# Performance work log

Hardware: AMD Instinct MI355X
Metric: run time of the kernel (lower is better)

## Reference

```python
import jax, jax.numpy as jnp
import numpy as np

N_NODES = 25000
N_EDGES = 400000
CHANNELS = 32
EDGE_FEAT_DIM = 8
HIDDEN = 64
NUM_IRREPS = 4  # messages irreps = 2x0e + 2x1o -> 4 irreps, dim 8
AVG_NUM_NEIGHBORS = 16.0


def _mlp(x, W0, W1, W2, W3):
    # e3nn MultiLayerPerceptron: dense layers with 1/sqrt(fan_in) forward
    # normalization, silu on hidden layers, no output activation.
    for W in (W0, W1, W2):
        x = jax.nn.silu(x @ (W / jnp.sqrt(jnp.float32(W.shape[0]))))
    return x @ (W3 / jnp.sqrt(jnp.float32(W3.shape[0])))


def setup_inputs() -> dict:
    key = jax.random.key(0)
    ks = jax.random.split(key, 9)
    node_feats = jax.random.normal(ks[0], (N_NODES, CHANNELS, 4), jnp.float32)
    edge_attrs = jax.random.normal(ks[1], (N_EDGES, 4), jnp.float32)
    edge_feats = jax.random.normal(ks[2], (N_EDGES, EDGE_FEAT_DIM), jnp.float32)
    senders = jax.random.randint(ks[3], (N_EDGES,), 0, N_NODES)
    receivers = jax.random.randint(ks[4], (N_EDGES,), 0, N_NODES)
    W0 = jax.random.normal(ks[5], (EDGE_FEAT_DIM, HIDDEN), jnp.float32)
    W1 = jax.random.normal(ks[6], (HIDDEN, HIDDEN), jnp.float32)
    W2 = jax.random.normal(ks[7], (HIDDEN, HIDDEN), jnp.float32)
    W3 = jax.random.normal(ks[8], (HIDDEN, CHANNELS * NUM_IRREPS), jnp.float32)
    return {"node_feats": node_feats, "edge_attrs": edge_attrs,
            "edge_feats": edge_feats, "senders": senders, "receivers": receivers,
            "W0": W0, "W1": W1, "W2": W2, "W3": W3}


def reference(node_feats, edge_attrs, edge_feats, senders, receivers, W0, W1, W2, W3):
    # Gather sender node features: [E, C, 4] with irreps 0e (dim1) + 1o (dim3)
    x = node_feats[senders]
    s, v = x[..., 0], x[..., 1:4]            # [E,C], [E,C,3]
    a_s = edge_attrs[:, 0]                   # Y_0: [E]
    a_v = edge_attrs[:, 1:4]                 # Y_1: [E,3]

    # CG tensor product filtered to 0e + 1o (e3nn normalization: sqrt(2l3+1)*w3j)
    m0a = s * a_s[:, None]                                   # 0e x 0e -> 0e  [E,C]
    m0b = jnp.einsum('ecd,ed->ec', v, a_v) / jnp.sqrt(3.0)   # 1o x 1o -> 0e  [E,C]
    m1a = s[..., None] * a_v[:, None, :]                     # 0e x 1o -> 1o  [E,C,3]
    m1b = v * a_s[:, None, None]                             # 1o x 0e -> 1o  [E,C,3]

    # Edge MLP gate: [E, C*num_irreps] -> mul_to_axis -> [E, C, num_irreps]
    mix = _mlp(edge_feats, W0, W1, W2, W3).reshape(N_EDGES, CHANNELS, NUM_IRREPS)

    # Elementwise tensor product with 4x0e scalars: per-irrep gating
    out_s = jnp.stack([m0a * mix[..., 0], m0b * mix[..., 1]], axis=-1)          # [E,C,2]
    out_v = jnp.concatenate([m1a * mix[..., 2:3], m1b * mix[..., 3:4]], axis=-1)  # [E,C,6]
    messages = jnp.concatenate([out_s, out_v], axis=-1)                          # [E,C,8]

    # Scatter-add into receivers, then normalize by sqrt(avg_num_neighbors)
    agg = jax.ops.segment_sum(messages, receivers, num_segments=N_NODES)
    return agg / jnp.sqrt(AVG_NUM_NEIGHBORS)
```

## Files before the change

kernel.cpp:

```cpp
#include <hip/hip_runtime.h>
#include <hip/hip_fp16.h>

#define NE 400000
#define NN 25000
#define MAXDEG 56
#define LDS_STRIDE 65

typedef __attribute__((ext_vector_type(8))) _Float16 half8;
typedef __attribute__((ext_vector_type(4))) _Float16 half4;
typedef __attribute__((ext_vector_type(4))) float f32x4;

#define WS_MIX_OFF   0ull
#define WS_SLOTS_OFF 102400000ull
#define WS_CNT_OFF   108000000ull
#define WS_WBUF_OFF  108100000ull
#define WS_NEED      108136864ull

#define WB_L0 0
#define WB_L1 2048
#define WB_L2 6144
#define WB_L3 10240

__device__ __forceinline__ float fast_silu(float x) {
    float e = __expf(-x);
    return x * __builtin_amdgcn_rcpf(1.0f + e);
}

__global__ __launch_bounds__(64) void prep_weights(
    const float* __restrict__ W0, const float* __restrict__ W1,
    const float* __restrict__ W2, const float* __restrict__ W3,
    _Float16* __restrict__ wbuf, int* __restrict__ cnt)
{
    const int f    = blockIdx.x;
    const int lane = threadIdx.x;

    for (int i = f * 64 + lane; i < NN; i += 36 * 64) cnt[i] = 0;

    const int n    = lane & 15;
    const int quad = lane >> 4;

    const float* W; int K, N, kt, nt, fl, base; float scale;
    if (f < 4)       { W = W0; K = 8;  N = 64;  fl = f;      kt = 0;       nt = fl;     scale = 0.35355339059327373f; base = WB_L0; }
    else if (f < 12) { W = W1; K = 64; N = 64;  fl = f - 4;  kt = fl >> 2; nt = fl & 3; scale = 0.125f;   base = WB_L1; }
    else if (f < 20) { W = W2; K = 64; N = 64;  fl = f - 12; kt = fl >> 2; nt = fl & 3; scale = 0.125f;   base = WB_L2; }
    else             { W = W3; K = 64; N = 128; fl = f - 20; kt = fl >> 3; nt = fl & 7; scale = 0.03125f; base = WB_L3; }

    _Float16 v[8];
    #pragma unroll
    for (int j = 0; j < 8; ++j) {
        const int k = kt * 32 + quad * 8 + j;
        const float val = (k < K) ? W[k * N + nt * 16 + n] * scale : 0.0f;
        v[j] = (_Float16)val;
    }
    *(half8*)(wbuf + base + fl * 512 + lane * 8) = *(const half8*)v;
}

#define HS 72
__global__ __launch_bounds__(256) void mlp_build_kernel(
    const float*    __restrict__ edge_feats,
    const int*      __restrict__ receivers,
    const _Float16* __restrict__ wbuf,
    int*            __restrict__ cnt,
    int*            __restrict__ slots,
    _Float16*       __restrict__ mix16)
{
    __shared__ _Float16 H[4 * 2 * 16 * HS];
    const int tid  = threadIdx.x;
    const int wave = tid >> 6;
    const int lane = tid & 63;
    const int col  = lane & 15;
    const int quad = lane >> 4;

    if (tid < 128) {
        const int e = blockIdx.x * 128 + tid;
        const int r = receivers[e];
        const int s = atomicAdd(&cnt[r], 1);
        if (s < MAXDEG) slots[r * MAXDEG + s] = e;
    }

    const int e0 = (blockIdx.x * 4 + wave) * 32;
    _Float16* HA = &H[wave * 2 * 16 * HS];
    _Float16* HB = HA + 16 * HS;
    const half8* wb = (const half8*)wbuf;
    const f32x4 zero4 = {0.f, 0.f, 0.f, 0.f};

    half8 b0A = {0, 0, 0, 0, 0, 0, 0, 0};
    half8 b0B = {0, 0, 0, 0, 0, 0, 0, 0};
    if (quad == 0) {
        const float4* pA = (const float4*)(edge_feats + (size_t)(e0 + col) * 8);
        const float4 xa = pA[0], ya = pA[1];
        b0A[0] = (_Float16)xa.x; b0A[1] = (_Float16)xa.y; b0A[2] = (_Float16)xa.z; b0A[3] = (_Float16)xa.w;
        b0A[4] = (_Float16)ya.x; b0A[5] = (_Float16)ya.y; b0A[6] = (_Float16)ya.z; b0A[7] = (_Float16)ya.w;
        const float4* pB = (const float4*)(edge_feats + (size_t)(e0 + 16 + col) * 8);
        const float4 xb = pB[0], yb = pB[1];
        b0B[0] = (_Float16)xb.x; b0B[1] = (_Float16)xb.y; b0B[2] = (_Float16)xb.z; b0B[3] = (_Float16)xb.w;
        b0B[4] = (_Float16)yb.x; b0B[5] = (_Float16)yb.y; b0B[6] = (_Float16)yb.z; b0B[7] = (_Float16)yb.w;
    }

    #pragma unroll
    for (int nt = 0; nt < 4; ++nt) {
        const half8 w = wb[(WB_L0 / 512 + nt) * 64 + lane];
        f32x4 aA = __builtin_amdgcn_mfma_f32_16x16x32_f16(w, b0A, zero4, 0, 0, 0);
        f32x4 aB = __builtin_amdgcn_mfma_f32_16x16x32_f16(w, b0B, zero4, 0, 0, 0);
        half4 hA, hB;
        #pragma unroll
        for (int r = 0; r < 4; ++r) { hA[r] = (_Float16)fast_silu(aA[r]); hB[r] = (_Float16)fast_silu(aB[r]); }
        *(half4*)&HA[col * HS + nt * 16 + quad * 4] = hA;
        *(half4*)&HB[col * HS + nt * 16 + quad * 4] = hB;
    }

    #pragma unroll
    for (int layer = 0; layer < 2; ++layer) {
        const int wbase = (layer == 0 ? WB_L1 : WB_L2) / 512;
        const half8 bloA = *(const half8*)&HA[col * HS + 0  + quad * 8];
        const half8 bhiA = *(const half8*)&HA[col * HS + 32 + quad * 8];
        const half8 bloB = *(const half8*)&HB[col * HS + 0  + quad * 8];
        const half8 bhiB = *(const half8*)&HB[col * HS + 32 + quad * 8];
        f32x4 aA[4], aB[4];
        #pragma unroll
        for (int nt = 0; nt < 4; ++nt) {
            const half8 wlo = wb[(wbase + 0 + nt) * 64 + lane];
            const half8 whi = wb[(wbase + 4 + nt) * 64 + lane];
            aA[nt] = __builtin_amdgcn_mfma_f32_16x16x32_f16(wlo, bloA, zero4, 0, 0, 0);
            aA[nt] = __builtin_amdgcn_mfma_f32_16x16x32_f16(whi, bhiA, aA[nt], 0, 0, 0);
            aB[nt] = __builtin_amdgcn_mfma_f32_16x16x32_f16(wlo, bloB, zero4, 0, 0, 0);
            aB[nt] = __builtin_amdgcn_mfma_f32_16x16x32_f16(whi, bhiB, aB[nt], 0, 0, 0);
        }
        #pragma unroll
        for (int nt = 0; nt < 4; ++nt) {
            half4 hA, hB;
            #pragma unroll
            for (int r = 0; r < 4; ++r) { hA[r] = (_Float16)fast_silu(aA[nt][r]); hB[r] = (_Float16)fast_silu(aB[nt][r]); }
            *(half4*)&HA[col * HS + nt * 16 + quad * 4] = hA;
            *(half4*)&HB[col * HS + nt * 16 + quad * 4] = hB;
        }
    }

    {
        const half8 bloA = *(const half8*)&HA[col * HS + 0  + quad * 8];
        const half8 bhiA = *(const half8*)&HA[col * HS + 32 + quad * 8];
        const half8 bloB = *(const half8*)&HB[col * HS + 0  + quad * 8];
        const half8 bhiB = *(const half8*)&HB[col * HS + 32 + quad * 8];
        _Float16* mrowA = mix16 + (size_t)(e0 + col) * 128;
        _Float16* mrowB = mix16 + (size_t)(e0 + 16 + col) * 128;
        #pragma unroll
        for (int nt = 0; nt < 8; ++nt) {
            const half8 wlo = wb[(WB_L3 / 512 + 0 + nt) * 64 + lane];
            const half8 whi = wb[(WB_L3 / 512 + 8 + nt) * 64 + lane];
            f32x4 aA = __builtin_amdgcn_mfma_f32_16x16x32_f16(wlo, bloA, zero4, 0, 0, 0);
            aA = __builtin_amdgcn_mfma_f32_16x16x32_f16(whi, bhiA, aA, 0, 0, 0);
            f32x4 aB = __builtin_amdgcn_mfma_f32_16x16x32_f16(wlo, bloB, zero4, 0, 0, 0);
            aB = __builtin_amdgcn_mfma_f32_16x16x32_f16(whi, bhiB, aB, 0, 0, 0);
            half4 hA, hB;
            #pragma unroll
            for (int r = 0; r < 4; ++r) { hA[r] = (_Float16)aA[r]; hB[r] = (_Float16)aB[r]; }
            *(half4*)&mrowA[nt * 16 + quad * 4] = hA;
            *(half4*)&mrowB[nt * 16 + quad * 4] = hB;
        }
    }
}

__global__ __launch_bounds__(64) void gather_kernel(
    const float*    __restrict__ node_feats,
    const float*    __restrict__ edge_attrs,
    const int*      __restrict__ senders,
    const _Float16* __restrict__ mix16,
    const int*      __restrict__ cnt,
    const int*      __restrict__ slots,
    float*          __restrict__ out)
{
    const int n    = blockIdx.x;
    const int lane = threadIdx.x;
    const int g    = lane >> 4;
    const int s    = lane & 15;
    const int c0   = 2 * s;
    const float inv_sqrt3 = 0.5773502691896258f;

    int d = cnt[n];
    if (d > MAXDEG) d = MAXDEG;
    const int* sl = slots + n * MAXDEG;

    float acc[16];
    #pragma unroll
    for (int j = 0; j < 16; ++j) acc[j] = 0.0f;

    #pragma unroll 2
    for (int base = 0; base < d; base += 4) {
        const int  ei  = base + g;
        const bool act = (ei < d);
        const int  eic = act ? ei : 0;
        const int  eid = sl[eic];
        const int  snd = senders[eid];
        const float4 a4v = ((const float4*)edge_attrs)[eid];
        const half8 m8 = *(const half8*)(mix16 + (size_t)eid * 128 + c0 * 4);
        const float4 xA = ((const float4*)(node_feats + (size_t)snd * 128))[c0];
        const float4 xB = ((const float4*)(node_feats + (size_t)snd * 128))[c0 + 1];

        const float z = act ? 1.0f : 0.0f;
        const float as = a4v.x, av0 = a4v.y, av1 = a4v.z, av2 = a4v.w;

        {
            const float m0 = z * (float)m8[0], m1 = z * (float)m8[1];
            const float m2 = z * (float)m8[2], m3 = z * (float)m8[3];
            const float sc = xA.x, v0 = xA.y, v1 = xA.z, v2 = xA.w;
            acc[0] = fmaf(sc * as, m0, acc[0]);
            const float dv = v0 * av0 + v1 * av1 + v2 * av2;
            acc[1] = fmaf(dv * inv_sqrt3, m1, acc[1]);
            acc[2] = fmaf(sc * av0, m2, acc[2]);
            acc[3] = fmaf(sc * av1, m2, acc[3]);
            acc[4] = fmaf(sc * av2, m2, acc[4]);
            acc[5] = fmaf(v0 * as, m3, acc[5]);
            acc[6] = fmaf(v1 * as, m3, acc[6]);
            acc[7] = fmaf(v2 * as, m3, acc[7]);
        }
        {
            const float m0 = z * (float)m8[4], m1 = z * (float)m8[5];
            const float m2 = z * (float)m8[6], m3 = z * (float)m8[7];
            const float sc = xB.x, v0 = xB.y, v1 = xB.z, v2 = xB.w;
            acc[8]  = fmaf(sc * as, m0, acc[8]);
            const float dv = v0 * av0 + v1 * av1 + v2 * av2;
            acc[9]  = fmaf(dv * inv_sqrt3, m1, acc[9]);
            acc[10] = fmaf(sc * av0, m2, acc[10]);
            acc[11] = fmaf(sc * av1, m2, acc[11]);
            acc[12] = fmaf(sc * av2, m2, acc[12]);
            acc[13] = fmaf(v0 * as, m3, acc[13]);
            acc[14] = fmaf(v1 * as, m3, acc[14]);
            acc[15] = fmaf(v2 * as, m3, acc[15]);
        }
    }

    #pragma unroll
    for (int j = 0; j < 16; ++j) {
        acc[j] += __shfl_xor(acc[j], 16, 64);
        acc[j] += __shfl_xor(acc[j], 32, 64);
    }

    if (g == 0) {
        float4* op = (float4*)(out + (size_t)n * 256 + s * 16);
        float4 r0; r0.x = acc[0];  r0.y = acc[1];  r0.z = acc[2];  r0.w = acc[3];
        float4 r1; r1.x = acc[4];  r1.y = acc[5];  r1.z = acc[6];  r1.w = acc[7];
        float4 r2; r2.x = acc[8];  r2.y = acc[9];  r2.z = acc[10]; r2.w = acc[11];
        float4 r3; r3.x = acc[12]; r3.y = acc[13]; r3.z = acc[14]; r3.w = acc[15];
        op[0] = r0; op[1] = r1; op[2] = r2; op[3] = r3;
    }
}

__global__ __launch_bounds__(128) void edge_mp_kernel(
    const float* __restrict__ node_feats, const float* __restrict__ edge_attrs,
    const float* __restrict__ edge_feats, const int* __restrict__ senders,
    const int* __restrict__ receivers, const float* __restrict__ W0,
    const float* __restrict__ W1, const float* __restrict__ W2,
    const float* __restrict__ W3, float* __restrict__ out)
{
    __shared__ float hbuf[128 * LDS_STRIDE];
    const int tid = threadIdx.x;
    const int e   = blockIdx.x * 128 + tid;
    if (e >= NE) return;
    float* hl = &hbuf[tid * LDS_STRIDE];

    float4 ef0 = ((const float4*)edge_feats)[e * 2 + 0];
    float4 ef1 = ((const float4*)edge_feats)[e * 2 + 1];
    float ef[8] = {ef0.x, ef0.y, ef0.z, ef0.w, ef1.x, ef1.y, ef1.z, ef1.w};
    float acc[64];
    #pragma unroll
    for (int i = 0; i < 64; ++i) acc[i] = 0.0f;
    #pragma unroll
    for (int j = 0; j < 8; ++j) {
        const float xj = ef[j];
        const float* wrow = W0 + j * 64;
        #pragma unroll
        for (int i = 0; i < 64; ++i) acc[i] = fmaf(xj, wrow[i], acc[i]);
    }
    {
        const float s0 = 0.35355339059327373f;
        #pragma unroll
        for (int i = 0; i < 64; ++i) hl[i] = fast_silu(acc[i] * s0);
    }
    #pragma unroll
    for (int i = 0; i < 64; ++i) acc[i] = 0.0f;
    #pragma unroll 4
    for (int j = 0; j < 64; ++j) {
        const float xj = hl[j];
        const float* wrow = W1 + j * 64;
        #pragma unroll
        for (int i = 0; i < 64; ++i) acc[i] = fmaf(xj, wrow[i], acc[i]);
    }
    #pragma unroll
    for (int i = 0; i < 64; ++i) hl[i] = fast_silu(acc[i] * 0.125f);
    #pragma unroll
    for (int i = 0; i < 64; ++i) acc[i] = 0.0f;
    #pragma unroll 4
    for (int j = 0; j < 64; ++j) {
        const float xj = hl[j];
        const float* wrow = W2 + j * 64;
        #pragma unroll
        for (int i = 0; i < 64; ++i) acc[i] = fmaf(xj, wrow[i], acc[i]);
    }
    float h2[64];
    #pragma unroll
    for (int i = 0; i < 64; ++i) h2[i] = fast_silu(acc[i] * 0.125f);

    const int snd = senders[e];
    const int rcv = receivers[e];
    const float4 a4 = ((const float4*)edge_attrs)[e];
    const float a_s = a4.x, av0 = a4.y, av1 = a4.z, av2 = a4.w;
    const float4* nf4 = (const float4*)(node_feats + (size_t)snd * 128);
    float* outp = out + (size_t)rcv * 256;
    const float mixscale = 0.03125f;
    const float inv_sqrt3 = 0.5773502691896258f;

    #pragma unroll 2
    for (int c = 0; c < 32; ++c) {
        float m0 = 0.0f, m1 = 0.0f, m2 = 0.0f, m3 = 0.0f;
        const float* wc = W3 + c * 4;
        #pragma unroll
        for (int j = 0; j < 64; ++j) {
            const float hj = h2[j];
            m0 = fmaf(hj, wc[j * 128 + 0], m0);
            m1 = fmaf(hj, wc[j * 128 + 1], m1);
            m2 = fmaf(hj, wc[j * 128 + 2], m2);
            m3 = fmaf(hj, wc[j * 128 + 3], m3);
        }
        m0 *= mixscale; m1 *= mixscale; m2 *= mixscale; m3 *= mixscale;
        const float4 x4 = nf4[c];
        const float s = x4.x, v0 = x4.y, v1 = x4.z, v2 = x4.w;
        float* op = outp + c * 8;
        atomicAdd(op + 0, s * a_s * m0);
        const float dotva = v0 * av0 + v1 * av1 + v2 * av2;
        atomicAdd(op + 1, dotva * inv_sqrt3 * m1);
        atomicAdd(op + 2, s * av0 * m2);
        atomicAdd(op + 3, s * av1 * m2);
        atomicAdd(op + 4, s * av2 * m2);
        atomicAdd(op + 5, v0 * a_s * m3);
        atomicAdd(op + 6, v1 * a_s * m3);
        atomicAdd(op + 7, v2 * a_s * m3);
    }
}

extern "C" void kernel_launch(void* const* d_in, const int* in_sizes, int n_in,
                              void* d_out, int out_size, void* d_ws, size_t ws_size,
                              hipStream_t stream) {
    const float* node_feats = (const float*)d_in[0];
    const float* edge_attrs = (const float*)d_in[1];
    const float* edge_feats = (const float*)d_in[2];
    const int*   senders    = (const int*)d_in[3];
    const int*   receivers  = (const int*)d_in[4];
    const float* W0 = (const float*)d_in[5];
    const float* W1 = (const float*)d_in[6];
    const float* W2 = (const float*)d_in[7];
    const float* W3 = (const float*)d_in[8];
    float* outp = (float*)d_out;

    if (ws_size >= WS_NEED) {
        char* w = (char*)d_ws;
        _Float16* mix16 = (_Float16*)(w + WS_MIX_OFF);
        int*      slots = (int*)(w + WS_SLOTS_OFF);
        int*      cnt   = (int*)(w + WS_CNT_OFF);
        _Float16* wbuf  = (_Float16*)(w + WS_WBUF_OFF);

        hipLaunchKernelGGL(prep_weights, dim3(36), dim3(64), 0, stream,
                           W0, W1, W2, W3, wbuf, cnt);
        hipLaunchKernelGGL(mlp_build_kernel, dim3(NE / 128), dim3(256), 0, stream,
                           edge_feats, receivers, wbuf, cnt, slots, mix16);
        hipLaunchKernelGGL(gather_kernel, dim3(NN), dim3(64), 0, stream,
                           node_feats, edge_attrs, senders, mix16, cnt, slots, outp);
    } else {
        hipMemsetAsync(d_out, 0, (size_t)out_size * sizeof(float), stream);
        hipLaunchKernelGGL(edge_mp_kernel, dim3((NE + 127) / 128), dim3(128), 0, stream,
                           node_feats, edge_attrs, edge_feats, senders, receivers,
                           W0, W1, W2, W3, outp);
    }
}
```

Baseline: 211.0 us.

## Make MLP kernel persistent with register-resident weights

The MLP/slot-building kernel becomes a persistent grid of 512 blocks that grid-stride over edge tiles and receiver-slot insertions. All 36 weight fragments are loaded into registers once per wave and reused across every tile, replacing per-tile weight reloads from global memory. Holding 36 half8 registers raises VGPR pressure, which the launch bound of 2 blocks per SM tries to contain. The cost is lower occupancy and possible load imbalance across the fixed grid.

After: 216.4 us. 1.03x slower.

```diff
diff --git a/kernel.cpp b/kernel.cpp
--- a/kernel.cpp
+++ b/kernel.cpp
@@ -5,6 +5,7 @@
 #define NN 25000
 #define MAXDEG 56
 #define LDS_STRIDE 65
+#define MLP_BLOCKS 512
 
 typedef __attribute__((ext_vector_type(8))) _Float16 half8;
 typedef __attribute__((ext_vector_type(4))) _Float16 half4;
@@ -56,7 +57,7 @@
 }
 
 #define HS 72
-__global__ __launch_bounds__(256) void mlp_build_kernel(
+__global__ __launch_bounds__(256, 2) void mlp_build_kernel(
     const float*    __restrict__ edge_feats,
     const int*      __restrict__ receivers,
     const _Float16* __restrict__ wbuf,
@@ -71,91 +72,93 @@
     const int col  = lane & 15;
     const int quad = lane >> 4;
 
-    if (tid < 128) {
-        const int e = blockIdx.x * 128 + tid;
+    for (int e = blockIdx.x * 256 + tid; e < NE; e += MLP_BLOCKS * 256) {
         const int r = receivers[e];
         const int s = atomicAdd(&cnt[r], 1);
         if (s < MAXDEG) slots[r * MAXDEG + s] = e;
     }
 
-    const int e0 = (blockIdx.x * 4 + wave) * 32;
+    const half8* wb = (const half8*)wbuf;
+    half8 w[36];
+    #pragma unroll
+    for (int i = 0; i < 36; ++i) w[i] = wb[i * 64 + lane];
+
     _Float16* HA = &H[wave * 2 * 16 * HS];
     _Float16* HB = HA + 16 * HS;
-    const half8* wb = (const half8*)wbuf;
     const f32x4 zero4 = {0.f, 0.f, 0.f, 0.f};
 
-    half8 b0A = {0, 0, 0, 0, 0, 0, 0, 0};
-    half8 b0B = {0, 0, 0, 0, 0, 0, 0, 0};
-    if (quad == 0) {
-        const float4* pA = (const float4*)(edge_feats + (size_t)(e0 + col) * 8);
-        const float4 xa = pA[0], ya = pA[1];
-        b0A[0] = (_Float16)xa.x; b0A[1] = (_Float16)xa.y; b0A[2] = (_Float16)xa.z; b0A[3] = (_Float16)xa.w;
-        b0A[4] = (_Float16)ya.x; b0A[5] = (_Float16)ya.y; b0A[6] = (_Float16)ya.z; b0A[7] = (_Float16)ya.w;
-        const float4* pB = (const float4*)(edge_feats + (size_t)(e0 + 16 + col) * 8);
-        const float4 xb = pB[0], yb = pB[1];
-        b0B[0] = (_Float16)xb.x; b0B[1] = (_Float16)xb.y; b0B[2] = (_Float16)xb.z; b0B[3] = (_Float16)xb.w;
-        b0B[4] = (_Float16)yb.x; b0B[5] = (_Float16)yb.y; b0B[6] = (_Float16)yb.z; b0B[7] = (_Float16)yb.w;
-    }
-
-    #pragma unroll
-    for (int nt = 0; nt < 4; ++nt) {
-        const half8 w = wb[(WB_L0 / 512 + nt) * 64 + lane];
-        f32x4 aA = __builtin_amdgcn_mfma_f32_16x16x32_f16(w, b0A, zero4, 0, 0, 0);
-        f32x4 aB = __builtin_amdgcn_mfma_f32_16x16x32_f16(w, b0B, zero4, 0, 0, 0);
-        half4 hA, hB;
-        #pragma unroll
-        for (int r = 0; r < 4; ++r) { hA[r] = (_Float16)fast_silu(aA[r]); hB[r] = (_Float16)fast_silu(aB[r]); }
-        *(half4*)&HA[col * HS + nt * 16 + quad * 4] = hA;
-        *(half4*)&HB[col * HS + nt * 16 + quad * 4] = hB;
-    }
-
-    #pragma unroll
-    for (int layer = 0; layer < 2; ++layer) {
-        const int wbase = (layer == 0 ? WB_L1 : WB_L2) / 512;
-        const half8 bloA = *(const half8*)&HA[col * HS + 0  + quad * 8];
-        const half8 bhiA = *(const half8*)&HA[col * HS + 32 + quad * 8];
-        const half8 bloB = *(const half8*)&HB[col * HS + 0  + quad * 8];
-        const half8 bhiB = *(const half8*)&HB[col * HS + 32 + quad * 8];
-        f32x4 aA[4], aB[4];
+    const int gw = blockIdx.x * 4 + wave;
+    for (int tp = gw; tp < NE / 32; tp += MLP_BLOCKS * 4) {
+        const int e0 = tp * 32;
+
+        half8 b0A = {0, 0, 0, 0, 0, 0, 0, 0};
+        half8 b0B = {0, 0, 0, 0, 0, 0, 0, 0};
+        if (quad == 0) {
+            const float4* pA = (const float4*)(edge_feats + (size_t)(e0 + col) * 8);
+            const float4 xa = pA[0], ya = pA[1];
+            b0A[0] = (_Float16)xa.x; b0A[1] = (_Float16)xa.y; b0A[2] = (_Float16)xa.z; b0A[3] = (_Float16)xa.w;
+            b0A[4] = (_Float16)ya.x; b0A[5] = (_Float16)ya.y; b0A[6] = (_Float16)ya.z; b0A[7] = (_Float16)ya.w;
+            const float4* pB = (const float4*)(edge_feats + (size_t)(e0 + 16 + col) * 8);
+            const float4 xb = pB[0], yb = pB[1];
+            b0B[0] = (_Float16)xb.x; b0B[1] = (_Float16)xb.y; b0B[2] = (_Float16)xb.z; b0B[3] = (_Float16)xb.w;
+            b0B[4] = (_Float16)yb.x; b0B[5] = (_Float16)yb.y; b0B[6] = (_Float16)yb.z; b0B[7] = (_Float16)yb.w;
+        }
+
         #pragma unroll
         for (int nt = 0; nt < 4; ++nt) {
-            const half8 wlo = wb[(wbase + 0 + nt) * 64 + lane];
-            const half8 whi = wb[(wbase + 4 + nt) * 64 + lane];
-            aA[nt] = __builtin_amdgcn_mfma_f32_16x16x32_f16(wlo, bloA, zero4, 0, 0, 0);
-            aA[nt] = __builtin_amdgcn_mfma_f32_16x16x32_f16(whi, bhiA, aA[nt], 0, 0, 0);
-            aB[nt] = __builtin_amdgcn_mfma_f32_16x16x32_f16(wlo, bloB, zero4, 0, 0, 0);
-            aB[nt] = __builtin_amdgcn_mfma_f32_16x16x32_f16(whi, bhiB, aB[nt], 0, 0, 0);
-        }
-        #pragma unroll
-        for (int nt = 0; nt < 4; ++nt) {
+            f32x4 aA = __builtin_amdgcn_mfma_f32_16x16x32_f16(w[nt], b0A, zero4, 0, 0, 0);
+            f32x4 aB = __builtin_amdgcn_mfma_f32_16x16x32_f16(w[nt], b0B, zero4, 0, 0, 0);
             half4 hA, hB;
             #pragma unroll
-            for (int r = 0; r < 4; ++r) { hA[r] = (_Float16)fast_silu(aA[nt][r]); hB[r] = (_Float16)fast_silu(aB[nt][r]); }
+            for (int r = 0; r < 4; ++r) { hA[r] = (_Float16)fast_silu(aA[r]); hB[r] = (_Float16)fast_silu(aB[r]); }
             *(half4*)&HA[col * HS + nt * 16 + quad * 4] = hA;
             *(half4*)&HB[col * HS + nt * 16 + quad * 4] = hB;
         }
-    }
-
-    {
-        const half8 bloA = *(const half8*)&HA[col * HS + 0  + quad * 8];
-        const half8 bhiA = *(const half8*)&HA[col * HS + 32 + quad * 8];
-        const half8 bloB = *(const half8*)&HB[col * HS + 0  + quad * 8];
-        const half8 bhiB = *(const half8*)&HB[col * HS + 32 + quad * 8];
-        _Float16* mrowA = mix16 + (size_t)(e0 + col) * 128;
-        _Float16* mrowB = mix16 + (size_t)(e0 + 16 + col) * 128;
-        #pragma unroll
-        for (int nt = 0; nt < 8; ++nt) {
-            const half8 wlo = wb[(WB_L3 / 512 + 0 + nt) * 64 + lane];
-            const half8 whi = wb[(WB_L3 / 512 + 8 + nt) * 64 + lane];
-            f32x4 aA = __builtin_amdgcn_mfma_f32_16x16x32_f16(wlo, bloA, zero4, 0, 0, 0);
-            aA = __builtin_amdgcn_mfma_f32_16x16x32_f16(whi, bhiA, aA, 0, 0, 0);
-            f32x4 aB = __builtin_amdgcn_mfma_f32_16x16x32_f16(wlo, bloB, zero4, 0, 0, 0);
-            aB = __builtin_amdgcn_mfma_f32_16x16x32_f16(whi, bhiB, aB, 0, 0, 0);
-            half4 hA, hB;
+
+        #pragma unroll
+        for (int layer = 0; layer < 2; ++layer) {
+            const int wo = (layer == 0) ? 4 : 12;
+            const half8 bloA = *(const half8*)&HA[col * HS + 0  + quad * 8];
+            const half8 bhiA = *(const half8*)&HA[col * HS + 32 + quad * 8];
+            const half8 bloB = *(const half8*)&HB[col * HS + 0  + quad * 8];
+            const half8 bhiB = *(const half8*)&HB[col * HS + 32 + quad * 8];
+            f32x4 aA[4], aB[4];
             #pragma unroll
-            for (int r = 0; r < 4; ++r) { hA[r] = (_Float16)aA[r]; hB[r] = (_Float16)aB[r]; }
-            *(half4*)&mrowA[nt * 16 + quad * 4] = hA;
-            *(half4*)&mrowB[nt * 16 + quad * 4] = hB;
+            for (int nt = 0; nt < 4; ++nt) {
+                aA[nt] = __builtin_amdgcn_mfma_f32_16x16x32_f16(w[wo + nt], bloA, zero4, 0, 0, 0);
+                aA[nt] = __builtin_amdgcn_mfma_f32_16x16x32_f16(w[wo + 4 + nt], bhiA, aA[nt], 0, 0, 0);
+                aB[nt] = __builtin_amdgcn_mfma_f32_16x16x32_f16(w[wo + nt], bloB, zero4, 0, 0, 0);
+                aB[nt] = __builtin_amdgcn_mfma_f32_16x16x32_f16(w[wo + 4 + nt], bhiB, aB[nt], 0, 0, 0);
+            }
+            #pragma unroll
+            for (int nt = 0; nt < 4; ++nt) {
+                half4 hA, hB;
+                #pragma unroll
+                for (int r = 0; r < 4; ++r) { hA[r] = (_Float16)fast_silu(aA[nt][r]); hB[r] = (_Float16)fast_silu(aB[nt][r]); }
+                *(half4*)&HA[col * HS + nt * 16 + quad * 4] = hA;
+                *(half4*)&HB[col * HS + nt * 16 + quad * 4] = hB;
+            }
+        }
+
+        {
+            const half8 bloA = *(const half8*)&HA[col * HS + 0  + quad * 8];
+            const half8 bhiA = *(const half8*)&HA[col * HS + 32 + quad * 8];
+            const half8 bloB = *(const half8*)&HB[col * HS + 0  + quad * 8];
+            const half8 bhiB = *(const half8*)&HB[col * HS + 32 + quad * 8];
+            _Float16* mrowA = mix16 + (size_t)(e0 + col) * 128;
+            _Float16* mrowB = mix16 + (size_t)(e0 + 16 + col) * 128;
+            #pragma unroll
+            for (int nt = 0; nt < 8; ++nt) {
+                f32x4 aA = __builtin_amdgcn_mfma_f32_16x16x32_f16(w[20 + nt], bloA, zero4, 0, 0, 0);
+                aA = __builtin_amdgcn_mfma_f32_16x16x32_f16(w[28 + nt], bhiA, aA, 0, 0, 0);
+                f32x4 aB = __builtin_amdgcn_mfma_f32_16x16x32_f16(w[20 + nt], bloB, zero4, 0, 0, 0);
+                aB = __builtin_amdgcn_mfma_f32_16x16x32_f16(w[28 + nt], bhiB, aB, 0, 0, 0);
+                half4 hA, hB;
+                #pragma unroll
+                for (int r = 0; r < 4; ++r) { hA[r] = (_Float16)aA[r]; hB[r] = (_Float16)aB[r]; }
+                *(half4*)&mrowA[nt * 16 + quad * 4] = hA;
+                *(half4*)&mrowB[nt * 16 + quad * 4] = hB;
+            }
         }
     }
 }
@@ -360,7 +363,7 @@
 
         hipLaunchKernelGGL(prep_weights, dim3(36), dim3(64), 0, stream,
                            W0, W1, W2, W3, wbuf, cnt);
-        hipLaunchKernelGGL(mlp_build_kernel, dim3(NE / 128), dim3(256), 0, stream,
+        hipLaunchKernelGGL(mlp_build_kernel, dim3(MLP_BLOCKS), dim3(256), 0, stream,
                            edge_feats, receivers, wbuf, cnt, slots, mix16);
         hipLaunchKernelGGL(gather_kernel, dim3(NN), dim3(64), 0, stream,
                            node_feats, edge_attrs, senders, mix16, cnt, slots, outp);
```
